# Kernel tuning notes

Measured on AMD Instinct MI355X. Metric: run time of the kernel, lower is better.

Reference implementation:

```python
import jax, jax.numpy as jnp
import numpy as np

IN_SIZE = 1024
OUT_SIZE = 1024
HEAD_NUM = 16
KEY_SIZE = OUT_SIZE // HEAD_NUM  # 64
MIN_VALUE = float(np.finfo(np.float32).min / 2.0)
LN_EPS = 1e-5


def setup_inputs() -> dict:
    key = jax.random.key(0)
    ks = jax.random.split(key, 12)
    B, L = 4, 1024
    s_in = 1.0 / np.sqrt(IN_SIZE)
    s_out = 1.0 / np.sqrt(OUT_SIZE)
    x = jax.random.normal(ks[0], (B, L, IN_SIZE), dtype=jnp.float32)
    mask = jax.random.randint(ks[1], (B, L), 0, 2, dtype=jnp.int32)
    # Per-head linears stacked: [H, in, key_size] (already transposed for x @ W)
    Wq = jax.random.normal(ks[2], (HEAD_NUM, IN_SIZE, KEY_SIZE), dtype=jnp.float32) * s_in
    bq = jax.random.normal(ks[3], (HEAD_NUM, KEY_SIZE), dtype=jnp.float32) * s_in
    Wk = jax.random.normal(ks[4], (HEAD_NUM, IN_SIZE, KEY_SIZE), dtype=jnp.float32) * s_in
    bk = jax.random.normal(ks[5], (HEAD_NUM, KEY_SIZE), dtype=jnp.float32) * s_in
    Wv = jax.random.normal(ks[6], (HEAD_NUM, IN_SIZE, KEY_SIZE), dtype=jnp.float32) * s_in
    bv = jax.random.normal(ks[7], (HEAD_NUM, KEY_SIZE), dtype=jnp.float32) * s_in
    Wo = jax.random.normal(ks[8], (OUT_SIZE, OUT_SIZE), dtype=jnp.float32) * s_out
    bo = jax.random.normal(ks[9], (OUT_SIZE,), dtype=jnp.float32) * s_out
    gamma = jnp.ones((OUT_SIZE,), dtype=jnp.float32)
    beta = jnp.zeros((OUT_SIZE,), dtype=jnp.float32)
    return {"x": x, "mask": mask, "Wq": Wq, "bq": bq, "Wk": Wk, "bk": bk,
            "Wv": Wv, "bv": bv, "Wo": Wo, "bo": bo, "gamma": gamma, "beta": beta}


def _attention(x, mask, Wq, bq, Wk, bk, Wv, bv, Wo, bo, gamma, beta):
    # Per-head projections, batched over heads: [B, H, L, d]
    q = jnp.einsum('bli,hid->bhld', x, Wq) + bq[None, :, None, :]
    k = jnp.einsum('bli,hid->bhld', x, Wk) + bk[None, :, None, :]
    v = jnp.einsum('bli,hid->bhld', x, Wv) + bv[None, :, None, :]
    scale = 1.0 / np.sqrt(KEY_SIZE)
    score = jnp.einsum('bhld,bhmd->bhlm', q, k) * scale  # [B, H, L, L]
    # masked_fill((mask == 0).unsqueeze(-2), min_value): mask over key positions
    score = jnp.where((mask == 0)[:, None, None, :], MIN_VALUE, score)
    atten = jax.nn.softmax(score, axis=-1)  # [B, H, L, L]
    value = jnp.einsum('bhlm,bhmd->bhld', atten, v)
    # concat heads -> [B, L, H*d] then output linear
    B, H, L, d = value.shape
    value = value.transpose(0, 2, 1, 3).reshape(B, L, H * d)
    value = value @ Wo.T + bo
    # wo_resize=False and in_size == out_size -> nearest interpolate is identity
    bypass = x
    pre = bypass + value
    mu = jnp.mean(pre, axis=-1, keepdims=True)
    var = jnp.mean(jnp.square(pre - mu), axis=-1, keepdims=True)
    out = (pre - mu) * jax.lax.rsqrt(var + LN_EPS) * gamma + beta
    return out, atten


def reference(x, mask, Wq, bq, Wk, bk, Wv, bv, Wo, bo, gamma, beta):
    return _attention(x, mask, Wq, bq, Wk, bk, Wv, bv, Wo, bo, gamma, beta)
```

## Files before the change

kernel.cpp:

```cpp
#include <hip/hip_runtime.h>
#include <hip/hip_bf16.h>

typedef __bf16 bf16x8 __attribute__((ext_vector_type(8)));
typedef __bf16 bf16x4 __attribute__((ext_vector_type(4)));
typedef float  f32x4  __attribute__((ext_vector_type(4)));

#define MIN_VALUE (-1.7014118346046923e38f)

__device__ __forceinline__ void async_load16(const __bf16* g, __bf16* l) {
    __builtin_amdgcn_global_load_lds(
        (const __attribute__((address_space(1))) uint32_t*)(uintptr_t)g,
        (__attribute__((address_space(3))) uint32_t*)(uint32_t)(uintptr_t)l,
        16, 0, 0);
}

__global__ __launch_bounds__(256) void conv_x_kernel(const float* __restrict__ x,
                                                     __bf16* __restrict__ xh) {
    int i = (blockIdx.x * 256 + threadIdx.x) * 4;
    float4 v = *(const float4*)(x + i);
    float vv[4] = {v.x, v.y, v.z, v.w};
    bf16x4 h;
    for (int e = 0; e < 4; ++e) h[e] = (__bf16)vv[e];
    *(bf16x4*)(xh + i) = h;
}

__global__ __launch_bounds__(256) void split_w_kernel(const float* __restrict__ Wq,
                                                      const float* __restrict__ Wk,
                                                      const float* __restrict__ Wv,
                                                      __bf16* __restrict__ wh,
                                                      __bf16* __restrict__ wl) {
    __shared__ float t[32][33];
    int z = blockIdx.z;
    int sel = z >> 4, h = z & 15;
    const float* W = (sel == 0) ? Wq : (sel == 1) ? Wk : Wv;
    int i0 = blockIdx.x * 32, d0 = blockIdx.y * 32;
    int tx = threadIdx.x & 31, ty = threadIdx.x >> 5;
    for (int it = 0; it < 4; ++it) {
        int r = ty + it * 8;
        t[r][tx] = W[(size_t)(h * 1024 + i0 + r) * 64 + d0 + tx];
    }
    __syncthreads();
    for (int it = 0; it < 4; ++it) {
        int r = ty + it * 8;
        float v = t[tx][r];
        size_t o = (size_t)(sel * 1024 + h * 64 + d0 + r) * 1024 + i0 + tx;
        __bf16 hi = (__bf16)v;
        wh[o] = hi;
        wl[o] = (__bf16)(v - (float)hi);
    }
}

__global__ __launch_bounds__(256) void conv_wo_kernel(const float* __restrict__ Wo,
                                                      __bf16* __restrict__ wob) {
    int i = (blockIdx.x * 256 + threadIdx.x) * 4;
    float4 v = *(const float4*)(Wo + i);
    float vv[4] = {v.x, v.y, v.z, v.w};
    bf16x4 h;
    for (int e = 0; e < 4; ++e) h[e] = (__bf16)vv[e];
    *(bf16x4*)(wob + i) = h;
}

__global__ __launch_bounds__(256) void qkv_gemm_kernel(
    const __bf16* __restrict__ xh,
    const __bf16* __restrict__ wh, const __bf16* __restrict__ wl,
    const float* __restrict__ bq, const float* __restrict__ bk, const float* __restrict__ bv,
    __bf16* __restrict__ qb, __bf16* __restrict__ kb, __bf16* __restrict__ vtb) {
    __shared__ __bf16 As[128 * 32];
    __shared__ __bf16 Bh[128 * 32];
    __shared__ __bf16 Bl[128 * 32];
    const int tid = threadIdx.x;
    const int m0 = blockIdx.y * 128;
    const int n0 = blockIdx.x * 128;
    const int lane = tid & 63, w = tid >> 6;
    const int l15 = lane & 15, quad = lane >> 4;
    const int wm = (w & 1) * 64, wn = (w >> 1) * 64;
    const int r4 = lane >> 2;
    const int c8 = (lane & 3) * 8;
    const bool need_lo = (n0 < 2048);

    f32x4 acc[4][4];
    for (int i = 0; i < 4; ++i)
        for (int j = 0; j < 4; ++j)
            for (int r = 0; r < 4; ++r) acc[i][j][r] = 0.0f;

    for (int kk = 0; kk < 1024; kk += 32) {
        __syncthreads();
        for (int half = 0; half < 2; ++half) {
            int row = w * 32 + half * 16 + r4;
            int lo = w * 1024 + half * 512 + lane * 8;
            async_load16(&xh[(size_t)(m0 + row) * 1024 + kk + c8], &As[lo]);
            async_load16(&wh[(size_t)(n0 + row) * 1024 + kk + c8], &Bh[lo]);
            if (need_lo)
                async_load16(&wl[(size_t)(n0 + row) * 1024 + kk + c8], &Bl[lo]);
        }
        __syncthreads();
        bf16x8 af[4], bhf[4], blf[4];
        for (int i = 0; i < 4; ++i)
            af[i] = *(const bf16x8*)&As[(wm + i * 16 + l15) * 32 + quad * 8];
        for (int j = 0; j < 4; ++j)
            bhf[j] = *(const bf16x8*)&Bh[(wn + j * 16 + l15) * 32 + quad * 8];
        if (need_lo)
            for (int j = 0; j < 4; ++j)
                blf[j] = *(const bf16x8*)&Bl[(wn + j * 16 + l15) * 32 + quad * 8];
        for (int i = 0; i < 4; ++i)
            for (int j = 0; j < 4; ++j)
                acc[i][j] = __builtin_amdgcn_mfma_f32_16x16x32_bf16(af[i], bhf[j], acc[i][j], 0, 0, 0);
        if (need_lo)
            for (int i = 0; i < 4; ++i)
                for (int j = 0; j < 4; ++j)
                    acc[i][j] = __builtin_amdgcn_mfma_f32_16x16x32_bf16(af[i], blf[j], acc[i][j], 0, 0, 0);
    }

    const int sel = n0 >> 10;
    const float* bias = (sel == 0) ? bq : (sel == 1) ? bk : bv;
    for (int i = 0; i < 4; ++i)
        for (int j = 0; j < 4; ++j)
            for (int r = 0; r < 4; ++r) {
                int m = m0 + wm + i * 16 + quad * 4 + r;
                int n = n0 + wn + j * 16 + l15;
                int nn = n & 1023;
                int h = nn >> 6, d = n & 63;
                float v = acc[i][j][r] + bias[nn];
                int bb = m >> 10, ll = m & 1023;
                if (sel == 2) {
                    vtb[(size_t)((bb * 16 + h) * 64 + d) * 1024 + ll] = (__bf16)v;
                } else {
                    __bf16* dst = (sel == 0) ? qb : kb;
                    dst[(size_t)((bb * 16 + h) * 1024 + ll) * 64 + d] = (__bf16)v;
                }
            }
}

__global__ __launch_bounds__(256, 4) void attn_kernel(
    const __bf16* __restrict__ qb, const __bf16* __restrict__ kb,
    const __bf16* __restrict__ vtb, const int* __restrict__ mask,
    float* __restrict__ atten, __bf16* __restrict__ value_bf) {
    __shared__ __bf16 P[16 * 1048];
    __shared__ float red[2][4][16];
    const int m0 = blockIdx.x * 16;
    const int h = blockIdx.y, b = blockIdx.z;
    const int bh = b * 16 + h;
    const int tid = threadIdx.x;
    const int lane = tid & 63, w = tid >> 6;
    const int l15 = lane & 15, quad = lane >> 4;

    const __bf16* qbase = qb + (size_t)(bh * 1024 + m0 + l15) * 64 + quad * 8;
    bf16x8 a0 = *(const bf16x8*)(qbase);
    bf16x8 a1 = *(const bf16x8*)(qbase + 32);
    f32x4 s[16];
    for (int t = 0; t < 16; ++t) {
        int n0 = w * 256 + t * 16;
        const __bf16* kbase = kb + (size_t)(bh * 1024 + n0 + l15) * 64 + quad * 8;
        bf16x8 b0 = *(const bf16x8*)(kbase);
        bf16x8 b1 = *(const bf16x8*)(kbase + 32);
        f32x4 c = {0.f, 0.f, 0.f, 0.f};
        c = __builtin_amdgcn_mfma_f32_16x16x32_bf16(a0, b0, c, 0, 0, 0);
        c = __builtin_amdgcn_mfma_f32_16x16x32_bf16(a1, b1, c, 0, 0, 0);
        bool msk = (mask[b * 1024 + n0 + l15] == 0);
        for (int r = 0; r < 4; ++r) s[t][r] = msk ? MIN_VALUE : c[r] * 0.125f;
    }

    float mx[4];
    for (int r = 0; r < 4; ++r) {
        float m = s[0][r];
        for (int t = 1; t < 16; ++t) m = fmaxf(m, s[t][r]);
        for (int o = 1; o < 16; o <<= 1) m = fmaxf(m, __shfl_xor(m, o));
        mx[r] = m;
    }
    if (l15 == 0)
        for (int r = 0; r < 4; ++r) red[0][w][quad * 4 + r] = mx[r];
    __syncthreads();
    for (int r = 0; r < 4; ++r) {
        int row = quad * 4 + r;
        mx[r] = fmaxf(fmaxf(red[0][0][row], red[0][1][row]),
                      fmaxf(red[0][2][row], red[0][3][row]));
    }

    float sum[4] = {0.f, 0.f, 0.f, 0.f};
    for (int t = 0; t < 16; ++t)
        for (int r = 0; r < 4; ++r) {
            float e = __expf(s[t][r] - mx[r]);
            s[t][r] = e;
            sum[r] += e;
            P[(quad * 4 + r) * 1048 + w * 256 + t * 16 + l15] = (__bf16)e;
        }
    for (int r = 0; r < 4; ++r) {
        float sm = sum[r];
        for (int o = 1; o < 16; o <<= 1) sm += __shfl_xor(sm, o);
        sum[r] = sm;
    }
    if (l15 == 0)
        for (int r = 0; r < 4; ++r) red[1][w][quad * 4 + r] = sum[r];
    __syncthreads();
    float inv[4];
    for (int r = 0; r < 4; ++r) {
        int row = quad * 4 + r;
        inv[r] = 1.0f / (red[1][0][row] + red[1][1][row] +
                         red[1][2][row] + red[1][3][row]);
    }

    for (int r = 0; r < 4; ++r) {
        float* out = atten + (size_t)(bh * 1024 + m0 + quad * 4 + r) * 1024 + w * 256 + l15;
        for (int t = 0; t < 16; ++t) out[t * 16] = s[t][r] * inv[r];
    }

    f32x4 acc = {0.f, 0.f, 0.f, 0.f};
    const __bf16* vbase = vtb + (size_t)(bh * 64 + w * 16 + l15) * 1024 + quad * 8;
    for (int kk = 0; kk < 1024; kk += 32) {
        bf16x8 af = *(const bf16x8*)&P[l15 * 1048 + kk + quad * 8];
        bf16x8 bf_ = *(const bf16x8*)(vbase + kk);
        acc = __builtin_amdgcn_mfma_f32_16x16x32_bf16(af, bf_, acc, 0, 0, 0);
    }
    for (int r = 0; r < 4; ++r) {
        int mrow = quad * 4 + r;
        value_bf[(size_t)(b * 1024 + m0 + mrow) * 1024 + h * 64 + w * 16 + l15] =
            (__bf16)(acc[r] * inv[r]);
    }
}

__global__ __launch_bounds__(256) void outproj_kernel(
    const __bf16* __restrict__ vb, const __bf16* __restrict__ wob,
    const float* __restrict__ x, const float* __restrict__ bo,
    float* __restrict__ pre) {
    __shared__ __bf16 As[128 * 32];
    __shared__ __bf16 Bs[128 * 32];
    const int tid = threadIdx.x;
    const int m0 = blockIdx.y * 128;
    const int n0 = blockIdx.x * 128;
    const int lane = tid & 63, w = tid >> 6;
    const int l15 = lane & 15, quad = lane >> 4;
    const int wm = (w & 1) * 64, wn = (w >> 1) * 64;
    const int r4 = lane >> 2;
    const int c8 = (lane & 3) * 8;

    f32x4 acc[4][4];
    for (int i = 0; i < 4; ++i)
        for (int j = 0; j < 4; ++j)
            for (int r = 0; r < 4; ++r) acc[i][j][r] = 0.0f;

    for (int kk = 0; kk < 1024; kk += 32) {
        __syncthreads();
        for (int half = 0; half < 2; ++half) {
            int row = w * 32 + half * 16 + r4;
            int lo = w * 1024 + half * 512 + lane * 8;
            async_load16(&vb[(size_t)(m0 + row) * 1024 + kk + c8], &As[lo]);
            async_load16(&wob[(size_t)(n0 + row) * 1024 + kk + c8], &Bs[lo]);
        }
        __syncthreads();
        bf16x8 af[4], bfr[4];
        for (int i = 0; i < 4; ++i) af[i] = *(const bf16x8*)&As[(wm + i * 16 + l15) * 32 + quad * 8];
        for (int j = 0; j < 4; ++j) bfr[j] = *(const bf16x8*)&Bs[(wn + j * 16 + l15) * 32 + quad * 8];
        for (int i = 0; i < 4; ++i)
            for (int j = 0; j < 4; ++j)
                acc[i][j] = __builtin_amdgcn_mfma_f32_16x16x32_bf16(af[i], bfr[j], acc[i][j], 0, 0, 0);
    }

    for (int i = 0; i < 4; ++i)
        for (int j = 0; j < 4; ++j)
            for (int r = 0; r < 4; ++r) {
                int m = m0 + wm + i * 16 + quad * 4 + r;
                int n = n0 + wn + j * 16 + l15;
                pre[(size_t)m * 1024 + n] = acc[i][j][r] + x[(size_t)m * 1024 + n] + bo[n];
            }
}

__global__ __launch_bounds__(256) void ln_kernel(float* __restrict__ buf,
                                                 const float* __restrict__ gamma,
                                                 const float* __restrict__ beta) {
    const int row = blockIdx.x;
    const int tid = threadIdx.x;
    const int lane = tid & 63, w = tid >> 6;
    __shared__ float red[8];
    float* rp = buf + (size_t)row * 1024;
    float loc[4];
    float s = 0.f, s2 = 0.f;
    for (int e = 0; e < 4; ++e) {
        loc[e] = rp[tid + e * 256];
        s += loc[e];
        s2 += loc[e] * loc[e];
    }
    for (int o = 32; o > 0; o >>= 1) {
        s += __shfl_xor(s, o);
        s2 += __shfl_xor(s2, o);
    }
    if (lane == 0) { red[w * 2] = s; red[w * 2 + 1] = s2; }
    __syncthreads();
    float ts = red[0] + red[2] + red[4] + red[6];
    float ts2 = red[1] + red[3] + red[5] + red[7];
    float mu = ts * (1.0f / 1024.0f);
    float var = ts2 * (1.0f / 1024.0f) - mu * mu;
    float sc = rsqrtf(var + 1e-5f);
    for (int e = 0; e < 4; ++e) {
        int c = tid + e * 256;
        rp[c] = (loc[e] - mu) * sc * gamma[c] + beta[c];
    }
}

extern "C" void kernel_launch(void* const* d_in, const int* in_sizes, int n_in,
                              void* d_out, int out_size, void* d_ws, size_t ws_size,
                              hipStream_t stream) {
    const float* x    = (const float*)d_in[0];
    const int*   mask = (const int*)d_in[1];
    const float* Wq   = (const float*)d_in[2];
    const float* bq   = (const float*)d_in[3];
    const float* Wk   = (const float*)d_in[4];
    const float* bk   = (const float*)d_in[5];
    const float* Wv   = (const float*)d_in[6];
    const float* bv   = (const float*)d_in[7];
    const float* Wo   = (const float*)d_in[8];
    const float* bo   = (const float*)d_in[9];
    const float* gamma= (const float*)d_in[10];
    const float* beta = (const float*)d_in[11];

    char* p = (char*)d_ws;
    __bf16* xh    = (__bf16*)p; p += (size_t)4194304 * 2;
    __bf16* wt_hi = (__bf16*)p; p += (size_t)3145728 * 2;
    __bf16* wt_lo = (__bf16*)p; p += (size_t)3145728 * 2;
    __bf16* wob   = (__bf16*)p; p += (size_t)1048576 * 2;
    __bf16* qb    = (__bf16*)p; p += (size_t)4194304 * 2;
    __bf16* kb    = (__bf16*)p; p += (size_t)4194304 * 2;
    __bf16* vtb   = (__bf16*)p; p += (size_t)4194304 * 2;
    __bf16* valb  = (__bf16*)p; p += (size_t)4194304 * 2;

    float* outb  = (float*)d_out;
    float* atten = outb + 4194304;

    conv_x_kernel<<<4096, 256, 0, stream>>>(x, xh);
    split_w_kernel<<<dim3(32, 2, 48), 256, 0, stream>>>(Wq, Wk, Wv, wt_hi, wt_lo);
    conv_wo_kernel<<<1024, 256, 0, stream>>>(Wo, wob);
    qkv_gemm_kernel<<<dim3(24, 32), 256, 0, stream>>>(xh, wt_hi, wt_lo, bq, bk, bv, qb, kb, vtb);
    attn_kernel<<<dim3(64, 16, 4), 256, 0, stream>>>(qb, kb, vtb, mask, atten, valb);
    outproj_kernel<<<dim3(8, 32), 256, 0, stream>>>(valb, wob, x, bo, outb);
    ln_kernel<<<4096, 256, 0, stream>>>(outb, gamma, beta);
}
```

Before: 520.9 us.

## Fuse prep kernels, coalesce attention-prob stores via LDS, halve outproj N tile

Merges the three input/weight conversion kernels into one launch dispatched by block index. The attention kernel now writes the normalized probability matrix by re-reading the bf16 P tile from shared memory and storing contiguous float4 rows, instead of strided scalar stores from registers. This changes the stored atten values to bf16-rounded precision. The output projection tile shrinks from 128x128 to 128x64, doubling the grid to 512 blocks so more CUs are used.

Result: faster. 500.6 us (-3.9%).

```diff
diff --git a/kernel.cpp b/kernel.cpp
--- a/kernel.cpp
+++ b/kernel.cpp
@@ -14,50 +14,50 @@
         16, 0, 0);
 }
 
-__global__ __launch_bounds__(256) void conv_x_kernel(const float* __restrict__ x,
-                                                     __bf16* __restrict__ xh) {
-    int i = (blockIdx.x * 256 + threadIdx.x) * 4;
-    float4 v = *(const float4*)(x + i);
-    float vv[4] = {v.x, v.y, v.z, v.w};
-    bf16x4 h;
-    for (int e = 0; e < 4; ++e) h[e] = (__bf16)vv[e];
-    *(bf16x4*)(xh + i) = h;
-}
-
-__global__ __launch_bounds__(256) void split_w_kernel(const float* __restrict__ Wq,
-                                                      const float* __restrict__ Wk,
-                                                      const float* __restrict__ Wv,
-                                                      __bf16* __restrict__ wh,
-                                                      __bf16* __restrict__ wl) {
+__global__ __launch_bounds__(256) void prep_kernel(
+    const float* __restrict__ x, const float* __restrict__ Wq,
+    const float* __restrict__ Wk, const float* __restrict__ Wv,
+    const float* __restrict__ Wo,
+    __bf16* __restrict__ xh, __bf16* __restrict__ wh, __bf16* __restrict__ wl,
+    __bf16* __restrict__ wob) {
     __shared__ float t[32][33];
-    int z = blockIdx.z;
-    int sel = z >> 4, h = z & 15;
-    const float* W = (sel == 0) ? Wq : (sel == 1) ? Wk : Wv;
-    int i0 = blockIdx.x * 32, d0 = blockIdx.y * 32;
-    int tx = threadIdx.x & 31, ty = threadIdx.x >> 5;
-    for (int it = 0; it < 4; ++it) {
-        int r = ty + it * 8;
-        t[r][tx] = W[(size_t)(h * 1024 + i0 + r) * 64 + d0 + tx];
-    }
-    __syncthreads();
-    for (int it = 0; it < 4; ++it) {
-        int r = ty + it * 8;
-        float v = t[tx][r];
-        size_t o = (size_t)(sel * 1024 + h * 64 + d0 + r) * 1024 + i0 + tx;
-        __bf16 hi = (__bf16)v;
-        wh[o] = hi;
-        wl[o] = (__bf16)(v - (float)hi);
-    }
-}
-
-__global__ __launch_bounds__(256) void conv_wo_kernel(const float* __restrict__ Wo,
-                                                      __bf16* __restrict__ wob) {
-    int i = (blockIdx.x * 256 + threadIdx.x) * 4;
-    float4 v = *(const float4*)(Wo + i);
-    float vv[4] = {v.x, v.y, v.z, v.w};
-    bf16x4 h;
-    for (int e = 0; e < 4; ++e) h[e] = (__bf16)vv[e];
-    *(bf16x4*)(wob + i) = h;
+    const int bid = blockIdx.x;
+    const int tid = threadIdx.x;
+    if (bid < 4096) {
+        int i = (bid * 256 + tid) * 4;
+        float4 v = *(const float4*)(x + i);
+        float vv[4] = {v.x, v.y, v.z, v.w};
+        bf16x4 h;
+        for (int e = 0; e < 4; ++e) h[e] = (__bf16)vv[e];
+        *(bf16x4*)(xh + i) = h;
+    } else if (bid < 5120) {
+        int i = ((bid - 4096) * 256 + tid) * 4;
+        float4 v = *(const float4*)(Wo + i);
+        float vv[4] = {v.x, v.y, v.z, v.w};
+        bf16x4 h;
+        for (int e = 0; e < 4; ++e) h[e] = (__bf16)vv[e];
+        *(bf16x4*)(wob + i) = h;
+    } else {
+        int b3 = bid - 5120;
+        int bx = b3 & 31, by = (b3 >> 5) & 1, z = b3 >> 6;
+        int sel = z >> 4, h = z & 15;
+        const float* W = (sel == 0) ? Wq : (sel == 1) ? Wk : Wv;
+        int i0 = bx * 32, d0 = by * 32;
+        int tx = tid & 31, ty = tid >> 5;
+        for (int it = 0; it < 4; ++it) {
+            int r = ty + it * 8;
+            t[r][tx] = W[(size_t)(h * 1024 + i0 + r) * 64 + d0 + tx];
+        }
+        __syncthreads();
+        for (int it = 0; it < 4; ++it) {
+            int r = ty + it * 8;
+            float v = t[tx][r];
+            size_t o = (size_t)(sel * 1024 + h * 64 + d0 + r) * 1024 + i0 + tx;
+            __bf16 hi = (__bf16)v;
+            wh[o] = hi;
+            wl[o] = (__bf16)(v - (float)hi);
+        }
+    }
 }
 
 __global__ __launch_bounds__(256) void qkv_gemm_kernel(
@@ -180,7 +180,6 @@
     for (int t = 0; t < 16; ++t)
         for (int r = 0; r < 4; ++r) {
             float e = __expf(s[t][r] - mx[r]);
-            s[t][r] = e;
             sum[r] += e;
             P[(quad * 4 + r) * 1048 + w * 256 + t * 16 + l15] = (__bf16)e;
         }
@@ -200,8 +199,16 @@
     }
 
     for (int r = 0; r < 4; ++r) {
-        float* out = atten + (size_t)(bh * 1024 + m0 + quad * 4 + r) * 1024 + w * 256 + l15;
-        for (int t = 0; t < 16; ++t) out[t * 16] = s[t][r] * inv[r];
+        int row = w * 4 + r;
+        float invr = 1.0f / (red[1][0][row] + red[1][1][row] +
+                             red[1][2][row] + red[1][3][row]);
+        float* out = atten + (size_t)(bh * 1024 + m0 + row) * 1024;
+        for (int e = 0; e < 4; ++e) {
+            bf16x4 pv = *(const bf16x4*)&P[row * 1048 + e * 256 + lane * 4];
+            f32x4 o;
+            for (int q2 = 0; q2 < 4; ++q2) o[q2] = (float)pv[q2] * invr;
+            *(f32x4*)(out + e * 256 + lane * 4) = o;
+        }
     }
 
     f32x4 acc = {0.f, 0.f, 0.f, 0.f};
@@ -223,19 +230,19 @@
     const float* __restrict__ x, const float* __restrict__ bo,
     float* __restrict__ pre) {
     __shared__ __bf16 As[128 * 32];
-    __shared__ __bf16 Bs[128 * 32];
+    __shared__ __bf16 Bs[64 * 32];
     const int tid = threadIdx.x;
     const int m0 = blockIdx.y * 128;
-    const int n0 = blockIdx.x * 128;
+    const int n0 = blockIdx.x * 64;
     const int lane = tid & 63, w = tid >> 6;
     const int l15 = lane & 15, quad = lane >> 4;
-    const int wm = (w & 1) * 64, wn = (w >> 1) * 64;
+    const int wm = (w & 1) * 64, wn = (w >> 1) * 32;
     const int r4 = lane >> 2;
     const int c8 = (lane & 3) * 8;
 
-    f32x4 acc[4][4];
+    f32x4 acc[4][2];
     for (int i = 0; i < 4; ++i)
-        for (int j = 0; j < 4; ++j)
+        for (int j = 0; j < 2; ++j)
             for (int r = 0; r < 4; ++r) acc[i][j][r] = 0.0f;
 
     for (int kk = 0; kk < 1024; kk += 32) {
@@ -244,19 +251,23 @@
             int row = w * 32 + half * 16 + r4;
             int lo = w * 1024 + half * 512 + lane * 8;
             async_load16(&vb[(size_t)(m0 + row) * 1024 + kk + c8], &As[lo]);
+        }
+        {
+            int row = w * 16 + r4;
+            int lo = w * 512 + lane * 8;
             async_load16(&wob[(size_t)(n0 + row) * 1024 + kk + c8], &Bs[lo]);
         }
         __syncthreads();
-        bf16x8 af[4], bfr[4];
+        bf16x8 af[4], bfr[2];
         for (int i = 0; i < 4; ++i) af[i] = *(const bf16x8*)&As[(wm + i * 16 + l15) * 32 + quad * 8];
-        for (int j = 0; j < 4; ++j) bfr[j] = *(const bf16x8*)&Bs[(wn + j * 16 + l15) * 32 + quad * 8];
+        for (int j = 0; j < 2; ++j) bfr[j] = *(const bf16x8*)&Bs[(wn + j * 16 + l15) * 32 + quad * 8];
         for (int i = 0; i < 4; ++i)
-            for (int j = 0; j < 4; ++j)
+            for (int j = 0; j < 2; ++j)
                 acc[i][j] = __builtin_amdgcn_mfma_f32_16x16x32_bf16(af[i], bfr[j], acc[i][j], 0, 0, 0);
     }
 
     for (int i = 0; i < 4; ++i)
-        for (int j = 0; j < 4; ++j)
+        for (int j = 0; j < 2; ++j)
             for (int r = 0; r < 4; ++r) {
                 int m = m0 + wm + i * 16 + quad * 4 + r;
                 int n = n0 + wn + j * 16 + l15;
@@ -325,11 +336,9 @@
     float* outb  = (float*)d_out;
     float* atten = outb + 4194304;
 
-    conv_x_kernel<<<4096, 256, 0, stream>>>(x, xh);
-    split_w_kernel<<<dim3(32, 2, 48), 256, 0, stream>>>(Wq, Wk, Wv, wt_hi, wt_lo);
-    conv_wo_kernel<<<1024, 256, 0, stream>>>(Wo, wob);
+    prep_kernel<<<8192, 256, 0, stream>>>(x, Wq, Wk, Wv, Wo, xh, wt_hi, wt_lo, wob);
     qkv_gemm_kernel<<<dim3(24, 32), 256, 0, stream>>>(xh, wt_hi, wt_lo, bq, bk, bv, qb, kb, vtb);
     attn_kernel<<<dim3(64, 16, 4), 256, 0, stream>>>(qb, kb, vtb, mask, atten, valb);
-    outproj_kernel<<<dim3(8, 32), 256, 0, stream>>>(valb, wob, x, bo, outb);
+    outproj_kernel<<<dim3(16, 32), 256, 0, stream>>>(valb, wob, x, bo, outb);
     ln_kernel<<<4096, 256, 0, stream>>>(outb, gamma, beta);
 }
```
